# Kernel tuning notes

Measured on AMD Instinct MI355X. Metric: run time of the kernel, lower is better.

## Reference

```python
import jax, jax.numpy as jnp
import numpy as np

NEG_SLOPE = 0.2  # PyG GATConv default
BN_EPS = 1e-5
NUM_GRAPHS = 128


def _bn(x, g, b, m, v):
    # eval-mode BatchNorm1d with running stats
    return (x - m) * jax.lax.rsqrt(v + BN_EPS) * g + b


def _gat_conv(x, src, dst, mask, W, a_src, a_dst, bias):
    # PyG GATConv: per-head linear, edge logits LeakyReLU(a_src.Wx_j + a_dst.Wx_i),
    # segment-softmax over incoming edges of each dst node, scatter-add messages.
    N = x.shape[0]
    H, C = a_src.shape
    xw = (x @ W).reshape(N, H, C)                       # [N,H,C]
    logit_s = (xw * a_src).sum(-1)                      # [N,H]
    logit_d = (xw * a_dst).sum(-1)                      # [N,H]
    e = jax.nn.leaky_relu(logit_s[src] + logit_d[dst], NEG_SLOPE)  # [E,H]
    e = jnp.where(mask[:, None], e, -1e30)              # edges filtered by edge_weights==1
    m = jax.ops.segment_max(e, dst, num_segments=N)     # [N,H]
    m = jnp.maximum(m, -1e30)                           # guard empty segments
    p = jnp.exp(e - m[dst]) * mask[:, None].astype(e.dtype)
    denom = jax.ops.segment_sum(p, dst, num_segments=N) + 1e-16
    alpha = p / denom[dst]                              # [E,H]
    out = jax.ops.segment_sum(xw[src] * alpha[..., None], dst, num_segments=N)
    return out.reshape(N, H * C) + bias


def setup_inputs() -> dict:
    key = jax.random.key(0)
    ks = jax.random.split(key, 20)
    N, E, F, G, NC = 20000, 320000, 128, NUM_GRAPHS, 10
    E0, E1, H = 256, 512, 2
    C = E1 // H

    def lin(k, fi, fo):
        return jax.random.normal(k, (fi, fo), jnp.float32) / np.float32(np.sqrt(fi))

    def bn(k, n):
        k1, k2, k3, k4 = jax.random.split(k, 4)
        g = 1.0 + 0.1 * jax.random.normal(k1, (n,), jnp.float32)
        b = 0.1 * jax.random.normal(k2, (n,), jnp.float32)
        m = 0.1 * jax.random.normal(k3, (n,), jnp.float32)
        v = 1.0 + 0.5 * jax.random.uniform(k4, (n,), jnp.float32)
        return g, b, m, v

    d = {}
    d['x'] = jax.random.normal(ks[0], (N, F), jnp.float32)
    d['edge_index'] = jax.random.randint(ks[1], (2, E), 0, N, dtype=jnp.int32)
    d['edge_weights'] = jnp.ones((E,), jnp.int32)
    d['batch'] = jnp.sort(jax.random.randint(ks[2], (N,), 0, G, dtype=jnp.int32))
    d['mlp_w1'] = lin(ks[3], F, E0); d['mlp_b1'] = jnp.zeros((E0,), jnp.float32)
    d['bn1_g'], d['bn1_b'], d['bn1_m'], d['bn1_v'] = bn(ks[4], E0)
    d['mlp_w2'] = lin(ks[5], E0, E0); d['mlp_b2'] = jnp.zeros((E0,), jnp.float32)
    d['bn2_g'], d['bn2_b'], d['bn2_m'], d['bn2_v'] = bn(ks[6], E0)
    d['gat0_w'] = lin(ks[7], E0, H * C)
    d['gat0_asrc'] = 0.1 * jax.random.normal(ks[8], (H, C), jnp.float32)
    d['gat0_adst'] = 0.1 * jax.random.normal(ks[9], (H, C), jnp.float32)
    d['gat0_bias'] = jnp.zeros((H * C,), jnp.float32)
    d['gat1_w'] = lin(ks[10], E1, H * C)
    d['gat1_asrc'] = 0.1 * jax.random.normal(ks[11], (H, C), jnp.float32)
    d['gat1_adst'] = 0.1 * jax.random.normal(ks[12], (H, C), jnp.float32)
    d['gat1_bias'] = jnp.zeros((H * C,), jnp.float32)
    d['bn3_g'], d['bn3_b'], d['bn3_m'], d['bn3_v'] = bn(ks[13], E1)
    d['fin_w1'] = lin(ks[14], E1, E1); d['fin_b1'] = jnp.zeros((E1,), jnp.float32)
    d['fin_w2'] = lin(ks[15], E1, NC); d['fin_b2'] = jnp.zeros((NC,), jnp.float32)
    return d


def reference(x, edge_index, edge_weights, batch,
              mlp_w1, mlp_b1, bn1_g, bn1_b, bn1_m, bn1_v,
              mlp_w2, mlp_b2, bn2_g, bn2_b, bn2_m, bn2_v,
              gat0_w, gat0_asrc, gat0_adst, gat0_bias,
              gat1_w, gat1_asrc, gat1_adst, gat1_bias,
              bn3_g, bn3_b, bn3_m, bn3_v,
              fin_w1, fin_b1, fin_w2, fin_b2):
    src, dst = edge_index[0], edge_index[1]
    mask = edge_weights == 1
    # initial MLP (dropout is identity in eval)
    h = jax.nn.relu(_bn(x @ mlp_w1 + mlp_b1, bn1_g, bn1_b, bn1_m, bn1_v))
    h = jax.nn.relu(_bn(h @ mlp_w2 + mlp_b2, bn2_g, bn2_b, bn2_m, bn2_v))
    # GAT layers
    h = _gat_conv(h, src, dst, mask, gat0_w, gat0_asrc, gat0_adst, gat0_bias)
    h = _gat_conv(h, src, dst, mask, gat1_w, gat1_asrc, gat1_adst, gat1_bias)
    # global mean pool over graphs
    sums = jax.ops.segment_sum(h, batch, num_segments=NUM_GRAPHS)
    cnt = jax.ops.segment_sum(jnp.ones((h.shape[0], 1), h.dtype), batch, num_segments=NUM_GRAPHS)
    pooled = sums / jnp.maximum(cnt, 1.0)
    # final head: BN -> ReLU -> Linear -> ReLU -> Linear
    z = jax.nn.relu(_bn(pooled, bn3_g, bn3_b, bn3_m, bn3_v))
    z = jax.nn.relu(z @ fin_w1 + fin_b1)
    return z @ fin_w2 + fin_b2
```

## Files before the change

### kernel.cpp

```cpp
#include <hip/hip_runtime.h>

typedef unsigned short u16;

constexpr int NN = 20000;
constexpr int EE = 320000;
constexpr int FD = 128;
constexpr int C0 = 256;
constexpr int C1 = 512;
constexpr int NG = 128;
constexpr int NC = 10;
constexpr int NBLK = (NN + 255) / 256;
constexpr int HB  = 320;
constexpr int EST = HB * 256;
constexpr int PSPL = 16;

constexpr size_t OFF_XB   = 0;
constexpr size_t OFF_H1   = OFF_XB  + (size_t)NN * FD * 2;
constexpr size_t OFF_H2   = OFF_H1  + (size_t)NN * C0 * 2;
constexpr size_t OFF_XW   = OFF_H2  + (size_t)NN * C0 * 2;
constexpr size_t OFF_H34  = OFF_XW  + (size_t)NN * C1 * 2;
constexpr size_t OFF_LS   = OFF_H34 + (size_t)NN * C1 * 2;
constexpr size_t OFF_LD   = OFF_LS  + (size_t)NN * 2 * 4;
constexpr size_t OFF_DEG  = OFF_LD  + (size_t)NN * 2 * 4;
constexpr size_t OFF_OFFS = OFF_DEG + (size_t)NN * 4;
constexpr size_t OFF_CUR  = OFF_OFFS + 80016;
constexpr size_t OFF_CSRC = OFF_CUR + (size_t)NN * 4;
constexpr size_t OFF_GCNT = OFF_CSRC + (size_t)EE * 4;
constexpr size_t OFF_GOFF = OFF_GCNT + 512;
constexpr size_t OFF_PART = OFF_GOFF + 768;
constexpr size_t OFF_PTOT = OFF_PART + 512;
constexpr size_t OFF_Z1   = OFF_PTOT + 256;
constexpr size_t OFF_Z2   = OFF_Z1  + (size_t)NG * C1 * 2;
constexpr size_t OFF_ST   = OFF_Z2  + (size_t)NG * C1 * 2;
constexpr size_t OFF_W1T  = OFF_ST  + 8192;
constexpr size_t OFF_W2T  = OFF_W1T + (size_t)FD * C0 * 2;
constexpr size_t OFF_G0T  = OFF_W2T + (size_t)C0 * C0 * 2;
constexpr size_t OFF_G1T  = OFF_G0T + (size_t)C0 * C1 * 2;
constexpr size_t OFF_AUX  = OFF_G1T + (size_t)C1 * C1 * 2;
constexpr size_t OFF_FLAG = OFF_AUX  + 0;
constexpr size_t OFF_A0S  = OFF_AUX  + 256;
constexpr size_t OFF_A0D  = OFF_AUX  + 1280;
constexpr size_t OFF_A1S  = OFF_AUX  + 2304;
constexpr size_t OFF_A1D  = OFF_AUX  + 3328;
constexpr size_t OFF_GB0  = OFF_AUX  + 4352;
constexpr size_t OFF_GB1  = OFF_AUX  + 6400;
constexpr size_t OFF_FB1  = OFF_AUX  + 8448;
constexpr size_t OFF_FB2  = OFF_AUX  + 10496;
constexpr size_t OFF_PP   = OFF_AUX  + 11008;
constexpr size_t OFF_DENA = OFF_PP + (size_t)NG * PSPL * C1 * 4;
constexpr size_t OFF_PLS  = OFF_DENA + (size_t)NN * 2 * 4;
constexpr size_t OFF_P0   = OFF_XB;
constexpr size_t OFF_P1   = OFF_XB + (size_t)EE * 4;

__device__ inline float bf2f(u16 u) { return __uint_as_float(((unsigned)u) << 16); }
__device__ inline u16 f2bf(float f) {
    unsigned u = __float_as_uint(f);
    unsigned r = u + 0x7fffu + ((u >> 16) & 1u);
    return (u16)(r >> 16);
}
__device__ inline float ldf(const void* p, long i, unsigned f) {
    return f ? ((const float*)p)[i] : bf2f(((const u16*)p)[i]);
}
__device__ inline void unpack8(uint4 r, float* v) {
    v[0] = __uint_as_float(r.x << 16); v[1] = __uint_as_float(r.x & 0xffff0000u);
    v[2] = __uint_as_float(r.y << 16); v[3] = __uint_as_float(r.y & 0xffff0000u);
    v[4] = __uint_as_float(r.z << 16); v[5] = __uint_as_float(r.z & 0xffff0000u);
    v[6] = __uint_as_float(r.w << 16); v[7] = __uint_as_float(r.w & 0xffff0000u);
}

typedef __bf16 bf16x8_t __attribute__((ext_vector_type(8)));
typedef float  f32x4_t  __attribute__((ext_vector_type(4)));

__device__ __forceinline__ void gl_lds16(const u16* g, u16* l) {
    __builtin_amdgcn_global_load_lds((const __attribute__((address_space(1))) void*)g,
                                     (__attribute__((address_space(3))) void*)l, 16, 0, 0);
}

__global__ void detect_dtype(const u16* __restrict__ x, const u16* __restrict__ w,
                             const u16* __restrict__ fw, unsigned* flag) {
    __shared__ int cnt;
    if (threadIdx.x == 0) cnt = 0;
    __syncthreads();
    int c = 0;
    for (int i = threadIdx.x; i < 4096; i += 256) {
        c += (((x[i]  >> 7) & 0xFF) == 0xFF);
        c += (((w[i]  >> 7) & 0xFF) == 0xFF);
        c += (((fw[i] >> 7) & 0xFF) == 0xFF);
    }
    atomicAdd(&cnt, c);
    __syncthreads();
    if (threadIdx.x == 0) *flag = (cnt >= 2) ? 1u : 0u;
}

__global__ void cvt_x(const unsigned* __restrict__ flag, const void* __restrict__ xin,
                      u16* __restrict__ XB, int* __restrict__ deg, int* __restrict__ gcnt) {
    int i = blockIdx.x * 256 + threadIdx.x;
    if (i < NN) deg[i] = 0;
    if (i < NG) gcnt[i] = 0;
    if (*flag) {
        float4 v = ((const float4*)xin)[i];
        ushort4 r;
        r.x = f2bf(v.x); r.y = f2bf(v.y); r.z = f2bf(v.z); r.w = f2bf(v.w);
        ((ushort4*)XB)[i] = r;
    } else {
        ((ushort4*)XB)[i] = ((const ushort4*)xin)[i];
    }
}

__global__ __launch_bounds__(512) void prep_trans(const unsigned* __restrict__ flag,
                            const void* g1, const void* b1, const void* m1, const void* v1, const void* lb1,
                            const void* g2, const void* b2, const void* m2, const void* v2, const void* lb2,
                            const void* g3, const void* b3, const void* m3, const void* v3,
                            const void* a0s, const void* a0d, const void* gb0in,
                            const void* a1s, const void* a1d, const void* gb1in,
                            const void* fb1in, const void* fb2in,
                            float* S1, float* T1, float* S2, float* T2, float* S3, float* T3,
                            u16* A0S, u16* A0D, u16* A1S, u16* A1D,
                            float* GB0, float* GB1, float* FB1, float* FB2,
                            const void* w1, const void* w2, const void* g0w, const void* g1w,
                            u16* w1T, u16* w2T, u16* g0T, u16* g1T) {
    unsigned f = *flag;
    if (blockIdx.x == 0) {
        int c = threadIdx.x;
        if (c < 256) {
            float s = ldf(g1, c, f) / sqrtf(ldf(v1, c, f) + 1e-5f);
            S1[c] = s; T1[c] = s * (ldf(lb1, c, f) - ldf(m1, c, f)) + ldf(b1, c, f);
            float s2 = ldf(g2, c, f) / sqrtf(ldf(v2, c, f) + 1e-5f);
            S2[c] = s2; T2[c] = s2 * (ldf(lb2, c, f) - ldf(m2, c, f)) + ldf(b2, c, f);
        }
        float s3 = ldf(g3, c, f) / sqrtf(ldf(v3, c, f) + 1e-5f);
        S3[c] = s3; T3[c] = ldf(b3, c, f) - ldf(m3, c, f) * s3;
        A0S[c] = f2bf(ldf(a0s, c, f));
        A0D[c] = f2bf(ldf(a0d, c, f));
        A1S[c] = f2bf(ldf(a1s, c, f));
        A1D[c] = f2bf(ldf(a1d, c, f));
        GB0[c] = ldf(gb0in, c, f);
        GB1[c] = ldf(gb1in, c, f);
        FB1[c] = ldf(fb1in, c, f);
        if (c < NC) FB2[c] = ldf(fb2in, c, f);
        return;
    }
    int b = blockIdx.x - 1;
    const void* B; u16* BT; int K, logN, base;
    if (b < 64)       { B = w1;  BT = w1T; K = FD; logN = 8; base = 0; }
    else if (b < 192) { B = w2;  BT = w2T; K = C0; logN = 8; base = 64; }
    else if (b < 448) { B = g0w; BT = g0T; K = C0; logN = 9; base = 192; }
    else              { B = g1w; BT = g1T; K = C1; logN = 9; base = 448; }
    int idx = (b - base) * 512 + threadIdx.x;
    int N = 1 << logN;
    int k = idx >> logN, n = idx & (N - 1);
    u16 v = f ? f2bf(((const float*)B)[idx]) : ((const u16*)B)[idx];
    BT[(size_t)n * K + k] = v;
}

__global__ __launch_bounds__(256) void hist_k(const int* __restrict__ dst, const int* __restrict__ ew,
                                              const int* __restrict__ batch,
                                              int* __restrict__ deg, int* __restrict__ gcnt) {
    int tid = blockIdx.x * 256 + threadIdx.x;
    int lane = threadIdx.x & 63;
#pragma unroll
    for (int j = 0; j < 4; j++) {
        int e = tid + j * EST;
        if (e < EE && ew[e] == 1) atomicAdd(&deg[dst[e]], 1);
    }
    int n = tid;
    if (n < NN) {
        int g = batch[n];
        int pg = __shfl_up(g, 1);
        bool head = (lane == 0) || (pg != g);
        unsigned long long act = __ballot(1);
        unsigned long long hm  = __ballot(head);
        if (head) {
            unsigned long long above = (lane < 63) ? ((hm >> (lane + 1)) << (lane + 1)) : 0ull;
            int limit = 64 - __builtin_clzll(act);
            int nxt = above ? __builtin_ctzll(above) : limit;
            atomicAdd(&gcnt[g], nxt - lane);
        }
    }
}
__global__ __launch_bounds__(256) void scan_blk(const int* __restrict__ deg, int* __restrict__ off,
                                                int* __restrict__ part) {
    __shared__ int tmp[256];
    int tid = threadIdx.x, i = blockIdx.x * 256 + tid;
    int v = (i < NN) ? deg[i] : 0;
    tmp[tid] = v;
    __syncthreads();
#pragma unroll
    for (int s = 1; s < 256; s <<= 1) {
        int a = (tid >= s) ? tmp[tid - s] : 0;
        __syncthreads();
        if (tid >= s) tmp[tid] += a;
        __syncthreads();
    }
    if (i < NN) off[i] = tmp[tid] - v;
    if (tid == 255) part[blockIdx.x] = tmp[255];
}
__global__ __launch_bounds__(128) void scan_small(int* __restrict__ part, int* __restrict__ ptot,
                                                  const int* __restrict__ gcnt, int* __restrict__ goff) {
    __shared__ int tmp[128];
    int tid = threadIdx.x;
    int v = (tid < NBLK) ? part[tid] : 0;
    tmp[tid] = v;
    __syncthreads();
#pragma unroll
    for (int s = 1; s < 128; s <<= 1) {
        int a = (tid >= s) ? tmp[tid - s] : 0;
        __syncthreads();
        if (tid >= s) tmp[tid] += a;
        __syncthreads();
    }
    if (tid < NBLK) part[tid] = tmp[tid] - v;
    if (tid == 127) *ptot = tmp[127];
    __syncthreads();
    int g = gcnt[tid];
    tmp[tid] = g;
    __syncthreads();
#pragma unroll
    for (int s = 1; s < 128; s <<= 1) {
        int a = (tid >= s) ? tmp[tid - s] : 0;
        __syncthreads();
        if (tid >= s) tmp[tid] += a;
        __syncthreads();
    }
    goff[tid] = tmp[tid] - g;
    if (tid == 127) goff[128] = tmp[127];
}
__global__ __launch_bounds__(256) void scan_add(int* __restrict__ off, const int* __restrict__ part,
                                                const int* __restrict__ ptot, int* __restrict__ cursor) {
    int tid = threadIdx.x, i = blockIdx.x * 256 + tid;
    if (i < NN) {
        int o = off[i] + part[blockIdx.x];
        off[i] = o;
        cursor[i] = o;
    }
    if (i == 0) off[NN] = *ptot;
}
__global__ __launch_bounds__(256) void csr_fill(const int* __restrict__ src, const int* __restrict__ dst,
                                                const int* __restrict__ ew,
                                                int* __restrict__ cursor, u16* __restrict__ csrc) {
    int tid = blockIdx.x * 256 + threadIdx.x;
    bool ok[4]; int sv[4]; int p[4];
#pragma unroll
    for (int j = 0; j < 4; j++) {
        int e = tid + j * EST;
        ok[j] = false; sv[j] = 0; p[j] = 0;
        if (e < EE && ew[e] == 1) {
            ok[j] = true;
            sv[j] = src[e];
            p[j] = atomicAdd(&cursor[dst[e]], 1);
        }
    }
#pragma unroll
    for (int j = 0; j < 4; j++) if (ok[j]) csrc[p[j]] = (u16)sv[j];
}

template <int EPI>
__global__ __launch_bounds__(256) void gemm_tile(const u16* __restrict__ A, const u16* __restrict__ BT,
                                                 u16* __restrict__ Cm,
                                                 const float* __restrict__ S, const float* __restrict__ T,
                                                 const u16* __restrict__ asrc, const u16* __restrict__ adst,
                                                 float2* __restrict__ pls,
                                                 int M, int N, int K) {
    __shared__ u16 As[128 * 64];
    __shared__ u16 Bs[128 * 64];
    const int tid  = threadIdx.x;
    const int wave = tid >> 6;
    const int lane = tid & 63;
    const int quad = lane >> 4;
    const int l16  = lane & 15;
    const int wr0  = (wave >> 1) * 64;
    const int wc0  = (wave & 1) * 64;
    const int row0 = blockIdx.x * 128;
    const int col0 = blockIdx.y * 128;

    const int srow = lane >> 3;
    const int sk   = ((lane & 7) ^ srow) * 8;
    const u16* gaP[4]; const u16* gbP[4]; u16* laP[4]; u16* lbP[4];
#pragma unroll
    for (int i = 0; i < 4; i++) {
        int rl = wave * 32 + i * 8 + srow;
        int gr = row0 + rl; if (gr >= M) gr = M - 1;
        gaP[i] = A  + (size_t)gr * K + sk;
        gbP[i] = BT + (size_t)(col0 + rl) * K + sk;
        laP[i] = As + (size_t)rl * 64 + (lane & 7) * 8;
        lbP[i] = Bs + (size_t)rl * 64 + (lane & 7) * 8;
    }

    f32x4_t acc[4][4];
#pragma unroll
    for (int r = 0; r < 4; r++)
#pragma unroll
        for (int c = 0; c < 4; c++)
#pragma unroll
            for (int i = 0; i < 4; i++) acc[r][c][i] = 0.f;

    for (int k0 = 0; k0 < K; k0 += 64) {
#pragma unroll
        for (int i = 0; i < 4; i++) {
            gl_lds16(gaP[i] + k0, laP[i]);
            gl_lds16(gbP[i] + k0, lbP[i]);
        }
        __syncthreads();

#pragma unroll
        for (int kk = 0; kk < 2; kk++) {
            bf16x8_t a[4], b[4];
#pragma unroll
            for (int r = 0; r < 4; r++) {
                int rr = wr0 + r * 16 + l16;
                a[r] = *(const bf16x8_t*)(As + (size_t)rr * 64 + (((kk * 4 + quad) ^ (rr & 7)) * 8));
            }
#pragma unroll
            for (int c = 0; c < 4; c++) {
                int cc = wc0 + c * 16 + l16;
                b[c] = *(const bf16x8_t*)(Bs + (size_t)cc * 64 + (((kk * 4 + quad) ^ (cc & 7)) * 8));
            }
#pragma unroll
            for (int r = 0; r < 4; r++)
#pragma unroll
                for (int c = 0; c < 4; c++)
                    acc[r][c] = __builtin_amdgcn_mfma_f32_16x16x32_bf16(a[r], b[c], acc[r][c], 0, 0, 0);
        }
        __syncthreads();
    }

    float2* lred = reinterpret_cast<float2*>(As);
#pragma unroll
    for (int r = 0; r < 4; r++) {
        int rb = row0 + wr0 + r * 16 + quad * 4;
        float ps[4] = {0.f, 0.f, 0.f, 0.f}, pd[4] = {0.f, 0.f, 0.f, 0.f};
#pragma unroll
        for (int c = 0; c < 4; c++) {
            int col = col0 + wc0 + c * 16 + l16;
            float sc = (EPI == 1) ? S[col] : 0.f;
            float sh = (EPI == 1) ? T[col] : 0.f;
            float av_ = 0.f, dv_ = 0.f;
            if (EPI == 3) { av_ = bf2f(asrc[col]); dv_ = bf2f(adst[col]); }
#pragma unroll
            for (int i = 0; i < 4; i++) {
                int row = rb + i;
                float v = acc[r][c][i];
                if (EPI == 1) v = fmaxf(v * sc + sh, 0.f);
                u16 bv = f2bf(v);
                if (row < M) Cm[(size_t)row * N + col] = bv;
                if (EPI == 3) {
                    float vb = bf2f(bv);
                    ps[i] = fmaf(vb, av_, ps[i]);
                    pd[i] = fmaf(vb, dv_, pd[i]);
                }
            }
        }
        if (EPI == 3) {
#pragma unroll
            for (int i = 0; i < 4; i++) {
#pragma unroll
                for (int m = 1; m <= 8; m <<= 1) {
                    ps[i] += __shfl_xor(ps[i], m);
                    pd[i] += __shfl_xor(pd[i], m);
                }
            }
            if (l16 == 0) {
#pragma unroll
                for (int i = 0; i < 4; i++) {
                    int rl = wr0 + r * 16 + quad * 4 + i;
                    lred[(size_t)(wave & 1) * 128 + rl] = make_float2(ps[i], pd[i]);
                }
            }
        }
    }
    if (EPI == 3) {
        __syncthreads();
        if (tid < 128) {
            int row = row0 + tid;
            if (row < M) {
                float2 a0 = lred[tid], a1 = lred[128 + tid];
                pls[(size_t)blockIdx.y * NN + row] = make_float2(a0.x + a1.x, a0.y + a1.y);
            }
        }
    }
}

__global__ __launch_bounds__(256) void ls_combine(const float2* __restrict__ pls,
                                                  float* __restrict__ ls, float* __restrict__ ld) {
    int n = blockIdx.x * 256 + threadIdx.x;
    if (n >= NN) return;
#pragma unroll
    for (int h = 0; h < 2; h++) {
        float2 a = pls[(size_t)(2 * h) * NN + n];
        float2 b = pls[(size_t)(2 * h + 1) * NN + n];
        ls[n * 2 + h] = a.x + b.x;
        ld[n * 2 + h] = a.y + b.y;
    }
}

__global__ __launch_bounds__(256) void gat_prep(const int* __restrict__ off, const u16* __restrict__ csrc,
                                                const float* __restrict__ ls, const float* __restrict__ ld,
                                                float* __restrict__ P0, float* __restrict__ P1,
                                                float* __restrict__ denA) {
    int n = blockIdx.x * 4 + (threadIdx.x >> 6);
    if (n >= NN) return;
    int lane = threadIdx.x & 63;
    int h = lane >> 5;
    int el = lane & 31;
    int beg = off[n], end = off[n + 1];
    float2 ldv = ((const float2*)ld)[n];
    float ldh = h ? ldv.y : ldv.x;
    float* __restrict__ Ph = h ? P1 : P0;
    float vmax = -1e30f;
    for (int base = beg; base < end; base += 32) {
        int e = base + el;
        int ec = e < end ? e : end - 1;
        int sv = csrc[ec];
        float vv = ls[sv * 2 + h] + ldh;
        vv = vv > 0.f ? vv : 0.2f * vv;
        if (e < end) vmax = fmaxf(vmax, vv);
    }
#pragma unroll
    for (int m = 16; m >= 1; m >>= 1) vmax = fmaxf(vmax, __shfl_xor(vmax, m));
    float mhat = vmax;
    float den = 0.f;
    for (int base = beg; base < end; base += 32) {
        int e = base + el;
        int ec = e < end ? e : end - 1;
        int sv = csrc[ec];
        float vv = ls[sv * 2 + h] + ldh;
        vv = vv > 0.f ? vv : 0.2f * vv;
        float p = __expf(vv - mhat);
        float pm = (e < end) ? p : 0.f;
#pragma unroll
        for (int m = 16; m >= 1; m >>= 1) pm += __shfl_xor(pm, m);
        den += pm;
        if (e < end) Ph[e] = p;
    }
    if (el == 0) denA[n * 2 + h] = den;
}

__device__ __forceinline__ void proc_edge(uint4 c, float w, float* acc) {
    float x[8];
    unpack8(c, x);
#pragma unroll
    for (int q = 0; q < 8; q++) acc[q] = fmaf(w, x[q], acc[q]);
}

__global__ __launch_bounds__(256) void gat_aggregate(const int* __restrict__ off, const u16* __restrict__ csrc,
                                                     const float* __restrict__ P0, const float* __restrict__ P1,
                                                     const float* __restrict__ denA,
                                                     const u16* __restrict__ xw,
                                                     const float* __restrict__ bias, u16* __restrict__ outh) {
    int n = blockIdx.x * 4 + (threadIdx.x >> 6);
    if (n >= NN) return;
    const int lane = threadIdx.x & 63;
    const int h    = lane >> 5;
    const int el   = lane & 31;
    const int hoff = h << 5;
    const float* __restrict__ Ph = h ? P1 : P0;
    int beg = off[n], end = off[n + 1];

    float acc[8];
#pragma unroll
    for (int q = 0; q < 8; q++) acc[q] = 0.f;

#define ROWLD(S) (((const uint4*)(xw + (size_t)(S) * C1))[lane])

    for (int base = beg; base < end; base += 32) {
        int cnt = end - base; if (cnt > 32) cnt = 32;
        int e = base + el;
        int ec = e < end ? e : end - 1;
        int sv = csrc[ec];
        float pv = Ph[ec];

        uint4 r0 = ROWLD(__shfl(sv, 0));
        uint4 r1 = ROWLD(__shfl(sv, 1));
        uint4 r2 = ROWLD(__shfl(sv, 2));
        uint4 r3 = ROWLD(__shfl(sv, 3));

        for (int j = 0; j < cnt; j += 4) {
            uint4 c0 = r0, c1 = r1, c2 = r2, c3 = r3;
            float w0 = __shfl(pv, j + hoff);
            float w1 = __shfl(pv, j + 1 + hoff);
            float w2 = __shfl(pv, j + 2 + hoff);
            float w3 = __shfl(pv, j + 3 + hoff);
            if (j + 4 < cnt) {
                r0 = ROWLD(__shfl(sv, j + 4));
                r1 = ROWLD(__shfl(sv, j + 5));
                r2 = ROWLD(__shfl(sv, j + 6));
                r3 = ROWLD(__shfl(sv, j + 7));
            }
            proc_edge(c0, w0, acc);
            if (j + 1 < cnt) proc_edge(c1, w1, acc);
            if (j + 2 < cnt) proc_edge(c2, w2, acc);
            if (j + 3 < cnt) proc_edge(c3, w3, acc);
        }
    }
#undef ROWLD

    float inv = 1.f / fmaxf(denA[n * 2 + h], 1e-30f);
    int cb = lane * 8;
    const float4* bp = (const float4*)(bias + cb);
    float4 b0 = bp[0], b1 = bp[1];
    uint4 st;
    st.x = (unsigned)f2bf(fmaf(acc[0], inv, b0.x)) | ((unsigned)f2bf(fmaf(acc[1], inv, b0.y)) << 16);
    st.y = (unsigned)f2bf(fmaf(acc[2], inv, b0.z)) | ((unsigned)f2bf(fmaf(acc[3], inv, b0.w)) << 16);
    st.z = (unsigned)f2bf(fmaf(acc[4], inv, b1.x)) | ((unsigned)f2bf(fmaf(acc[5], inv, b1.y)) << 16);
    st.w = (unsigned)f2bf(fmaf(acc[6], inv, b1.z)) | ((unsigned)f2bf(fmaf(acc[7], inv, b1.w)) << 16);
    ((uint4*)(outh + (size_t)n * C1 + cb))[0] = st;
}

__global__ __launch_bounds__(128) void pool_part(const u16* __restrict__ h4, const int* __restrict__ goff,
                                                 float* __restrict__ pp) {
    int g = blockIdx.x, s = blockIdx.y, t = threadIdx.x;
    int b = goff[g], e = goff[g + 1];
    int len = e - b;
    int chunk = (len + PSPL - 1) / PSPL;
    int n0 = b + s * chunk;
    int n1 = n0 + chunk; if (n1 > e) n1 = e;
    float s0 = 0.f, s1 = 0.f, s2 = 0.f, s3 = 0.f;
    for (int n = n0; n < n1; n++) {
        ushort4 v = *(const ushort4*)(h4 + (size_t)n * C1 + t * 4);
        s0 += bf2f(v.x); s1 += bf2f(v.y); s2 += bf2f(v.z); s3 += bf2f(v.w);
    }
    float4* dst = (float4*)(pp + ((size_t)g * PSPL + s) * C1 + t * 4);
    *dst = make_float4(s0, s1, s2, s3);
}

__global__ __launch_bounds__(512) void head_all(const unsigned* __restrict__ flag,
                                                const float* __restrict__ pp, const int* __restrict__ goff,
                                                const float* __restrict__ S3, const float* __restrict__ T3,
                                                const void* __restrict__ w1, const float* __restrict__ FB1,
                                                const void* __restrict__ w2, const float* __restrict__ FB2,
                                                void* __restrict__ out) {
    __shared__ float zrow[512];
    __shared__ float z2row[512];
    __shared__ float red[512];
    int g = blockIdx.x, t = threadIdx.x;
    unsigned f = *flag;
    float s = 0.f;
#pragma unroll
    for (int k = 0; k < PSPL; k++) s += pp[((size_t)g * PSPL + k) * C1 + t];
    int b = goff[g], e = goff[g + 1];
    float mean = s / fmaxf((float)(e - b), 1.f);
    float v = fmaxf(mean * S3[t] + T3[t], 0.f);
    zrow[t] = bf2f(f2bf(v));
    __syncthreads();
    float acc = 0.f;
    if (f) {
        const float* w = (const float*)w1;
        for (int k = 0; k < 512; k++) acc = fmaf(zrow[k], w[(size_t)k * 512 + t], acc);
    } else {
        const u16* w = (const u16*)w1;
        for (int k = 0; k < 512; k++) acc = fmaf(zrow[k], bf2f(w[(size_t)k * 512 + t]), acc);
    }
    acc += FB1[t];
    z2row[t] = bf2f(f2bf(fmaxf(acc, 0.f)));
    __syncthreads();
    float z2t = z2row[t];
    for (int o = 0; o < NC; o++) {
        float p = f ? z2t * ((const float*)w2)[(size_t)t * NC + o]
                    : z2t * bf2f(((const u16*)w2)[(size_t)t * NC + o]);
        red[t] = p;
        __syncthreads();
#pragma unroll
        for (int sd = 256; sd >= 1; sd >>= 1) {
            if (t < sd) red[t] += red[t + sd];
            __syncthreads();
        }
        if (t == 0) {
            float vv = red[0] + FB2[o];
            if (f) ((float*)out)[g * NC + o] = vv;
            else   ((u16*)out)[g * NC + o] = f2bf(vv);
        }
        __syncthreads();
    }
}

extern "C" void kernel_launch(void* const* d_in, const int* in_sizes, int n_in,
                              void* d_out, int out_size, void* d_ws, size_t ws_size,
                              hipStream_t stream) {
    (void)in_sizes; (void)n_in; (void)out_size; (void)ws_size;

    const void* x      = d_in[0];
    const int* ei      = (const int*)d_in[1];
    const int* src     = ei;
    const int* dst     = ei + EE;
    const int* ew      = (const int*)d_in[2];
    const int* batch   = (const int*)d_in[3];
    const void* mlp_w1 = d_in[4];
    const void* mlp_b1 = d_in[5];
    const void *bn1g = d_in[6], *bn1b = d_in[7], *bn1m = d_in[8], *bn1v = d_in[9];
    const void* mlp_w2 = d_in[10];
    const void* mlp_b2 = d_in[11];
    const void *bn2g = d_in[12], *bn2b = d_in[13], *bn2m = d_in[14], *bn2v = d_in[15];
    const void* g0w    = d_in[16];
    const void* g0as   = d_in[17];
    const void* g0ad   = d_in[18];
    const void* g0bias = d_in[19];
    const void* g1w    = d_in[20];
    const void* g1as   = d_in[21];
    const void* g1ad   = d_in[22];
    const void* g1bias = d_in[23];
    const void *bn3g = d_in[24], *bn3b = d_in[25], *bn3m = d_in[26], *bn3v = d_in[27];
    const void* fin_w1 = d_in[28];
    const void* fin_b1 = d_in[29];
    const void* fin_w2 = d_in[30];
    const void* fin_b2 = d_in[31];

    char* ws = (char*)d_ws;
    u16*  XB   = (u16*)(ws + OFF_XB);
    u16*  h1   = (u16*)(ws + OFF_H1);
    u16*  h2   = (u16*)(ws + OFF_H2);
    u16*  xw   = (u16*)(ws + OFF_XW);
    u16*  h34  = (u16*)(ws + OFF_H34);
    float* ls  = (float*)(ws + OFF_LS);
    float* ld  = (float*)(ws + OFF_LD);
    int*  deg  = (int*)(ws + OFF_DEG);
    int*  off  = (int*)(ws + OFF_OFFS);
    int*  cur  = (int*)(ws + OFF_CUR);
    u16*  csrc = (u16*)(ws + OFF_CSRC);
    int*  gcnt = (int*)(ws + OFF_GCNT);
    int*  goff = (int*)(ws + OFF_GOFF);
    int*  part = (int*)(ws + OFF_PART);
    int*  ptot = (int*)(ws + OFF_PTOT);
    float* S1 = (float*)(ws + OFF_ST);
    float* T1 = S1 + 256;
    float* S2 = T1 + 256;
    float* T2 = S2 + 256;
    float* S3 = T2 + 256;
    float* T3 = S3 + 512;
    u16* w1T = (u16*)(ws + OFF_W1T);
    u16* w2T = (u16*)(ws + OFF_W2T);
    u16* g0T = (u16*)(ws + OFF_G0T);
    u16* g1T = (u16*)(ws + OFF_G1T);
    unsigned* flag = (unsigned*)(ws + OFF_FLAG);
    u16* A0S = (u16*)(ws + OFF_A0S);
    u16* A0D = (u16*)(ws + OFF_A0D);
    u16* A1S = (u16*)(ws + OFF_A1S);
    u16* A1D = (u16*)(ws + OFF_A1D);
    float* GB0 = (float*)(ws + OFF_GB0);
    float* GB1 = (float*)(ws + OFF_GB1);
    float* FB1 = (float*)(ws + OFF_FB1);
    float* FB2 = (float*)(ws + OFF_FB2);
    float* PP = (float*)(ws + OFF_PP);
    float* DENA = (float*)(ws + OFF_DENA);
    float2* PLS = (float2*)(ws + OFF_PLS);
    float* P0 = (float*)(ws + OFF_P0);
    float* P1 = (float*)(ws + OFF_P1);

    detect_dtype<<<1, 256, 0, stream>>>((const u16*)x, (const u16*)mlp_w1, (const u16*)fin_w1, flag);
    cvt_x<<<(NN * FD / 4) / 256, 256, 0, stream>>>(flag, x, XB, deg, gcnt);
    prep_trans<<<961, 512, 0, stream>>>(flag,
                                        bn1g, bn1b, bn1m, bn1v, mlp_b1,
                                        bn2g, bn2b, bn2m, bn2v, mlp_b2,
                                        bn3g, bn3b, bn3m, bn3v,
                                        g0as, g0ad, g0bias, g1as, g1ad, g1bias,
                                        fin_b1, fin_b2,
                                        S1, T1, S2, T2, S3, T3,
                                        A0S, A0D, A1S, A1D, GB0, GB1, FB1, FB2,
                                        mlp_w1, mlp_w2, g0w, g1w, w1T, w2T, g0T, g1T);

    hist_k<<<HB, 256, 0, stream>>>(dst, ew, batch, deg, gcnt);
    scan_blk<<<NBLK, 256, 0, stream>>>(deg, off, part);
    scan_small<<<1, 128, 0, stream>>>(part, ptot, gcnt, goff);
    scan_add<<<NBLK, 256, 0, stream>>>(off, part, ptot, cur);
    csr_fill<<<HB, 256, 0, stream>>>(src, dst, ew, cur, csrc);

    gemm_tile<1><<<dim3(157, 2), 256, 0, stream>>>(XB, w1T, h1, S1, T1, nullptr, nullptr, nullptr, NN, C0, FD);
    gemm_tile<1><<<dim3(157, 2), 256, 0, stream>>>(h1, w2T, h2, S2, T2, nullptr, nullptr, nullptr, NN, C0, C0);

    gemm_tile<3><<<dim3(157, 4), 256, 0, stream>>>(h2, g0T, xw, nullptr, nullptr, A0S, A0D, PLS, NN, C1, C0);
    ls_combine<<<NBLK, 256, 0, stream>>>(PLS, ls, ld);
    gat_prep<<<NN / 4, 256, 0, stream>>>(off, csrc, ls, ld, P0, P1, DENA);
    gat_aggregate<<<NN / 4, 256, 0, stream>>>(off, csrc, P0, P1, DENA, xw, GB0, h34);

    gemm_tile<3><<<dim3(157, 4), 256, 0, stream>>>(h34, g1T, xw, nullptr, nullptr, A1S, A1D, PLS, NN, C1, C1);
    ls_combine<<<NBLK, 256, 0, stream>>>(PLS, ls, ld);
    gat_prep<<<NN / 4, 256, 0, stream>>>(off, csrc, ls, ld, P0, P1, DENA);
    gat_aggregate<<<NN / 4, 256, 0, stream>>>(off, csrc, P0, P1, DENA, xw, GB1, h34);

    pool_part<<<dim3(NG, PSPL), 128, 0, stream>>>(h34, goff, PP);
    head_all<<<NG, 512, 0, stream>>>(flag, PP, goff, S3, T3, fin_w1, FB1, fin_w2, FB2, d_out);
}
```

Measured before the change: 380.7 us.

## Fuse GAT softmax prep into aggregation and recompute edge weights in-register

Merges the softmax-prep kernel into the aggregation kernel. Each wavefront now computes the max and the denominator, then recomputes the exponentiated edge weights while aggregating, instead of writing per-edge P arrays and a denominator buffer to global memory and reading them back. This removes the P0/P1/denA round trip and the prep kernel, at the cost of a third gather pass over ls and extra exp work per edge. The fused kernel is also launched as two half-node-range launches per layer, which adds a launch and drops the bounds check.

New measurement: 377.6 us. No clear change (-0.8%).

```diff
diff --git a/kernel.cpp b/kernel.cpp
--- a/kernel.cpp
+++ b/kernel.cpp
@@ -49,8 +49,6 @@
 constexpr size_t OFF_PP   = OFF_AUX  + 11008;
 constexpr size_t OFF_DENA = OFF_PP + (size_t)NG * PSPL * C1 * 4;
 constexpr size_t OFF_PLS  = OFF_DENA + (size_t)NN * 2 * 4;
-constexpr size_t OFF_P0   = OFF_XB;
-constexpr size_t OFF_P1   = OFF_XB + (size_t)EE * 4;
 
 __device__ inline float bf2f(u16 u) { return __uint_as_float(((unsigned)u) << 16); }
 __device__ inline u16 f2bf(float f) {
@@ -393,19 +391,27 @@
     }
 }
 
-__global__ __launch_bounds__(256) void gat_prep(const int* __restrict__ off, const u16* __restrict__ csrc,
-                                                const float* __restrict__ ls, const float* __restrict__ ld,
-                                                float* __restrict__ P0, float* __restrict__ P1,
-                                                float* __restrict__ denA) {
-    int n = blockIdx.x * 4 + (threadIdx.x >> 6);
-    if (n >= NN) return;
-    int lane = threadIdx.x & 63;
-    int h = lane >> 5;
-    int el = lane & 31;
+__device__ __forceinline__ void proc_edge(uint4 c, float w, float* acc) {
+    float x[8];
+    unpack8(c, x);
+#pragma unroll
+    for (int q = 0; q < 8; q++) acc[q] = fmaf(w, x[q], acc[q]);
+}
+
+template <int HALF>
+__global__ __launch_bounds__(256) void gat_agg_fused(const int* __restrict__ off, const u16* __restrict__ csrc,
+                                                     const float* __restrict__ ls, const float* __restrict__ ld,
+                                                     const u16* __restrict__ xw,
+                                                     const float* __restrict__ bias, u16* __restrict__ outh) {
+    int n = HALF * (NN / 2) + blockIdx.x * 4 + (threadIdx.x >> 6);
+    const int lane = threadIdx.x & 63;
+    const int h    = lane >> 5;
+    const int el   = lane & 31;
+    const int hoff = h << 5;
     int beg = off[n], end = off[n + 1];
     float2 ldv = ((const float2*)ld)[n];
     float ldh = h ? ldv.y : ldv.x;
-    float* __restrict__ Ph = h ? P1 : P0;
+
     float vmax = -1e30f;
     for (int base = beg; base < end; base += 32) {
         int e = base + el;
@@ -417,7 +423,8 @@
     }
 #pragma unroll
     for (int m = 16; m >= 1; m >>= 1) vmax = fmaxf(vmax, __shfl_xor(vmax, m));
-    float mhat = vmax;
+    const float mhat = vmax;
+
     float den = 0.f;
     for (int base = beg; base < end; base += 32) {
         int e = base + el;
@@ -430,31 +437,7 @@
 #pragma unroll
         for (int m = 16; m >= 1; m >>= 1) pm += __shfl_xor(pm, m);
         den += pm;
-        if (e < end) Ph[e] = p;
-    }
-    if (el == 0) denA[n * 2 + h] = den;
-}
-
-__device__ __forceinline__ void proc_edge(uint4 c, float w, float* acc) {
-    float x[8];
-    unpack8(c, x);
-#pragma unroll
-    for (int q = 0; q < 8; q++) acc[q] = fmaf(w, x[q], acc[q]);
-}
-
-__global__ __launch_bounds__(256) void gat_aggregate(const int* __restrict__ off, const u16* __restrict__ csrc,
-                                                     const float* __restrict__ P0, const float* __restrict__ P1,
-                                                     const float* __restrict__ denA,
-                                                     const u16* __restrict__ xw,
-                                                     const float* __restrict__ bias, u16* __restrict__ outh) {
-    int n = blockIdx.x * 4 + (threadIdx.x >> 6);
-    if (n >= NN) return;
-    const int lane = threadIdx.x & 63;
-    const int h    = lane >> 5;
-    const int el   = lane & 31;
-    const int hoff = h << 5;
-    const float* __restrict__ Ph = h ? P1 : P0;
-    int beg = off[n], end = off[n + 1];
+    }
 
     float acc[8];
 #pragma unroll
@@ -467,7 +450,9 @@
         int e = base + el;
         int ec = e < end ? e : end - 1;
         int sv = csrc[ec];
-        float pv = Ph[ec];
+        float vv = ls[sv * 2 + h] + ldh;
+        vv = vv > 0.f ? vv : 0.2f * vv;
+        float myp = __expf(vv - mhat);
 
         uint4 r0 = ROWLD(__shfl(sv, 0));
         uint4 r1 = ROWLD(__shfl(sv, 1));
@@ -476,10 +461,10 @@
 
         for (int j = 0; j < cnt; j += 4) {
             uint4 c0 = r0, c1 = r1, c2 = r2, c3 = r3;
-            float w0 = __shfl(pv, j + hoff);
-            float w1 = __shfl(pv, j + 1 + hoff);
-            float w2 = __shfl(pv, j + 2 + hoff);
-            float w3 = __shfl(pv, j + 3 + hoff);
+            float w0 = __shfl(myp, j + hoff);
+            float w1 = __shfl(myp, j + 1 + hoff);
+            float w2 = __shfl(myp, j + 2 + hoff);
+            float w3 = __shfl(myp, j + 3 + hoff);
             if (j + 4 < cnt) {
                 r0 = ROWLD(__shfl(sv, j + 4));
                 r1 = ROWLD(__shfl(sv, j + 5));
@@ -494,7 +479,7 @@
     }
 #undef ROWLD
 
-    float inv = 1.f / fmaxf(denA[n * 2 + h], 1e-30f);
+    float inv = 1.f / fmaxf(den, 1e-30f);
     int cb = lane * 8;
     const float4* bp = (const float4*)(bias + cb);
     float4 b0 = bp[0], b1 = bp[1];
@@ -640,10 +625,7 @@
     float* FB1 = (float*)(ws + OFF_FB1);
     float* FB2 = (float*)(ws + OFF_FB2);
     float* PP = (float*)(ws + OFF_PP);
-    float* DENA = (float*)(ws + OFF_DENA);
     float2* PLS = (float2*)(ws + OFF_PLS);
-    float* P0 = (float*)(ws + OFF_P0);
-    float* P1 = (float*)(ws + OFF_P1);
 
     detect_dtype<<<1, 256, 0, stream>>>((const u16*)x, (const u16*)mlp_w1, (const u16*)fin_w1, flag);
     cvt_x<<<(NN * FD / 4) / 256, 256, 0, stream>>>(flag, x, XB, deg, gcnt);
@@ -668,13 +650,13 @@
 
     gemm_tile<3><<<dim3(157, 4), 256, 0, stream>>>(h2, g0T, xw, nullptr, nullptr, A0S, A0D, PLS, NN, C1, C0);
     ls_combine<<<NBLK, 256, 0, stream>>>(PLS, ls, ld);
-    gat_prep<<<NN / 4, 256, 0, stream>>>(off, csrc, ls, ld, P0, P1, DENA);
-    gat_aggregate<<<NN / 4, 256, 0, stream>>>(off, csrc, P0, P1, DENA, xw, GB0, h34);
+    gat_agg_fused<0><<<(NN / 2) / 4, 256, 0, stream>>>(off, csrc, ls, ld, xw, GB0, h34);
+    gat_agg_fused<1><<<(NN / 2) / 4, 256, 0, stream>>>(off, csrc, ls, ld, xw, GB0, h34);
 
     gemm_tile<3><<<dim3(157, 4), 256, 0, stream>>>(h34, g1T, xw, nullptr, nullptr, A1S, A1D, PLS, NN, C1, C1);
     ls_combine<<<NBLK, 256, 0, stream>>>(PLS, ls, ld);
-    gat_prep<<<NN / 4, 256, 0, stream>>>(off, csrc, ls, ld, P0, P1, DENA);
-    gat_aggregate<<<NN / 4, 256, 0, stream>>>(off, csrc, P0, P1, DENA, xw, GB1, h34);
+    gat_agg_fused<0><<<(NN / 2) / 4, 256, 0, stream>>>(off, csrc, ls, ld, xw, GB1, h34);
+    gat_agg_fused<1><<<(NN / 2) / 4, 256, 0, stream>>>(off, csrc, ls, ld, xw, GB1, h34);
 
     pool_part<<<dim3(NG, PSPL), 128, 0, stream>>>(h34, goff, PP);
     head_all<<<NG, 512, 0, stream>>>(flag, PP, goff, S3, T3, fin_w1, FB1, fin_w2, FB2, d_out);
```
